# Performance work log

Measured on AMD Instinct MI355X. Metric: run time of the kernel, lower is better.

Reference implementation:

```python
import jax, jax.numpy as jnp
import numpy as np

D_MODEL = 1024
HEADS = 16
D_HEAD = D_MODEL // HEADS


def setup_inputs() -> dict:
    key = jax.random.key(0)
    ks = jax.random.split(key, 7)
    s = 1.0 / np.sqrt(D_MODEL)
    x = jax.random.normal(ks[0], (4, 2048, D_MODEL), dtype=jnp.float32)
    Wq = jax.random.uniform(ks[1], (D_MODEL, D_MODEL), jnp.float32, -s, s)
    bq = jax.random.uniform(ks[2], (D_MODEL,), jnp.float32, -s, s)
    Wk = jax.random.uniform(ks[3], (D_MODEL, D_MODEL), jnp.float32, -s, s)
    bk = jax.random.uniform(ks[4], (D_MODEL,), jnp.float32, -s, s)
    Wv = jax.random.uniform(ks[5], (D_MODEL, D_MODEL), jnp.float32, -s, s)
    bv = jax.random.uniform(ks[6], (D_MODEL,), jnp.float32, -s, s)
    return {"x": x, "Wq": Wq, "bq": bq, "Wk": Wk, "bk": bk, "Wv": Wv, "bv": bv}


def reference(x, Wq, bq, Wk, bk, Wv, bv):
    B, S, D = x.shape
    # QKV projections, split heads: [B, H, S, Dh]
    def split(t):
        return t.reshape(B, S, HEADS, D_HEAD).transpose(0, 2, 1, 3)
    q = split(x @ Wq + bq)
    k = split(x @ Wk + bk)
    v = split(x @ Wv + bv)
    scores = jnp.einsum('bhqd,bhkd->bhqk', q, k) / np.sqrt(D_HEAD).astype(jnp.float32)
    attn = jax.nn.softmax(scores, axis=-1)
    out = jnp.einsum('bhqk,bhkd->bhqd', attn, v)
    return out.transpose(0, 2, 1, 3).reshape(B, S, D)
```

## Files before the change

kernel.cpp:

```cpp
#include <hip/hip_runtime.h>

typedef _Float16 f16;
typedef __attribute__((ext_vector_type(2))) _Float16 f16x2;
typedef __attribute__((ext_vector_type(2))) __fp16   hf16x2;
typedef __attribute__((ext_vector_type(4))) _Float16 f16x4;
typedef __attribute__((ext_vector_type(8))) _Float16 f16x8;
typedef __attribute__((ext_vector_type(4))) float    f32x4;

#define D_MODEL 1024
#define HEADS   16
#define DH      64
#define SEQ     2048
#define BATCH   4
#define SSCALE  0.1803368801111204f

__device__ __forceinline__ void gload_lds16(const void* g, void* lds) {
  __builtin_amdgcn_global_load_lds(
      (const __attribute__((address_space(1))) unsigned int*)g,
      (__attribute__((address_space(3))) unsigned int*)lds, 16, 0, 0);
}

__global__ __launch_bounds__(256) void prep_kernel(const float* __restrict__ x,
                                                   const float* __restrict__ Wq,
                                                   const float* __restrict__ Wk,
                                                   const float* __restrict__ Wv,
                                                   f16* __restrict__ xb,
                                                   f16* __restrict__ wt) {
  if (blockIdx.x < 8192) {
    int i = blockIdx.x * 256 + threadIdx.x;
    float4 v = ((const float4*)x)[i];
    f16x4 h;
    h[0] = (f16)v.x; h[1] = (f16)v.y; h[2] = (f16)v.z; h[3] = (f16)v.w;
    ((f16x4*)xb)[i] = h;
    return;
  }
  int bid = blockIdx.x - 8192;
  int z = bid >> 8, rem = bid & 255;
  const float* W = z == 0 ? Wq : (z == 1 ? Wk : Wv);
  f16* out = wt + (size_t)z * D_MODEL * D_MODEL;
  __shared__ float tile[64][65];
  int n0 = (rem & 15) * 64, k0 = (rem >> 4) * 64;
  int tx = threadIdx.x & 63, ty = threadIdx.x >> 6;
#pragma unroll
  for (int r = 0; r < 16; ++r)
    tile[ty * 16 + r][tx] = W[(size_t)(k0 + ty * 16 + r) * D_MODEL + n0 + tx];
  __syncthreads();
#pragma unroll
  for (int r = 0; r < 16; ++r)
    out[(size_t)(n0 + ty * 16 + r) * D_MODEL + k0 + tx] = (f16)tile[tx][ty * 16 + r];
}

__global__ __launch_bounds__(256, 3) void qkv_gemm_kernel(
    const f16* __restrict__ xb, const f16* __restrict__ wt_all,
    const float* __restrict__ bq, const float* __restrict__ bk, const float* __restrict__ bv,
    f16* __restrict__ qout, f16* __restrict__ kout, f16* __restrict__ vtout) {
  const int z = blockIdx.z;
  const f16* wt = wt_all + (size_t)z * D_MODEL * D_MODEL;
  const float* bias = z == 0 ? bq : (z == 1 ? bk : bv);
  const int n0 = blockIdx.x * 128, m0 = blockIdx.y * 128;

  __shared__ f16 As[2][128 * 32];
  __shared__ f16 Bs[2][128 * 32];

  const int tid = threadIdx.x;
  const int lane = tid & 63, w = tid >> 6;
  const int quad = lane >> 4, l15 = lane & 15;
  const int wm = w & 1, wn = w >> 1;

  const int pce = (quad ^ ((l15 >> 1) & 3)) * 8;
  const int aoff = wm * 2048 + l15 * 32 + pce;
  const int boff = wn * 2048 + l15 * 32 + pce;

  int srow[2], scl[2];
#pragma unroll
  for (int c = 0; c < 2; ++c) {
    int slot = (w * 2 + c) * 64 + lane;
    srow[c] = slot >> 2;
    scl[c] = (slot & 3) ^ ((srow[c] >> 1) & 3);
  }

  f32x4 acc[4][4];
#pragma unroll
  for (int i = 0; i < 4; ++i)
#pragma unroll
    for (int j = 0; j < 4; ++j) acc[i][j] = (f32x4){0.f, 0.f, 0.f, 0.f};

#pragma unroll
  for (int c = 0; c < 2; ++c) {
    gload_lds16(xb + (size_t)(m0 + srow[c]) * D_MODEL + scl[c] * 8, &As[0][(w * 2 + c) * 512]);
    gload_lds16(wt + (size_t)(n0 + srow[c]) * D_MODEL + scl[c] * 8, &Bs[0][(w * 2 + c) * 512]);
  }

  f16x8 aP[4], bP[4];
  for (int it = 0; it < 32; ++it) {
    const int buf = it & 1;
    __syncthreads();
    if (it < 31) {
      const int kn = (it + 1) * 32;
#pragma unroll
      for (int c = 0; c < 2; ++c) {
        gload_lds16(xb + (size_t)(m0 + srow[c]) * D_MODEL + kn + scl[c] * 8, &As[buf ^ 1][(w * 2 + c) * 512]);
        gload_lds16(wt + (size_t)(n0 + srow[c]) * D_MODEL + kn + scl[c] * 8, &Bs[buf ^ 1][(w * 2 + c) * 512]);
      }
    }
    f16x8 aC[4], bC[4];
#pragma unroll
    for (int mt = 0; mt < 4; ++mt) aC[mt] = *(const f16x8*)(&As[buf][aoff + mt * 512]);
#pragma unroll
    for (int nt = 0; nt < 4; ++nt) bC[nt] = *(const f16x8*)(&Bs[buf][boff + nt * 512]);
    if (it) {
#pragma unroll
      for (int mt = 0; mt < 4; ++mt)
#pragma unroll
        for (int nt = 0; nt < 4; ++nt)
          acc[mt][nt] = __builtin_amdgcn_mfma_f32_16x16x32_f16(aP[mt], bP[nt], acc[mt][nt], 0, 0, 0);
    }
#pragma unroll
    for (int t = 0; t < 4; ++t) { aP[t] = aC[t]; bP[t] = bC[t]; }
  }
#pragma unroll
  for (int mt = 0; mt < 4; ++mt)
#pragma unroll
    for (int nt = 0; nt < 4; ++nt)
      acc[mt][nt] = __builtin_amdgcn_mfma_f32_16x16x32_f16(aP[mt], bP[nt], acc[mt][nt], 0, 0, 0);

  const float sc = (z == 0) ? SSCALE : 1.0f;
  float bcol[4];
#pragma unroll
  for (int nt = 0; nt < 4; ++nt) bcol[nt] = bias[n0 + wn * 64 + nt * 16 + l15];

  if (z < 2) {
    f16* out = (z == 0) ? qout : kout;
#pragma unroll
    for (int mt = 0; mt < 4; ++mt) {
      int mbase = m0 + wm * 64 + mt * 16 + quad * 4;
#pragma unroll
      for (int nt = 0; nt < 4; ++nt) {
        int n = n0 + wn * 64 + nt * 16 + l15;
        int h = n >> 6, dh = n & 63;
#pragma unroll
        for (int r = 0; r < 4; ++r) {
          int m = mbase + r;
          int b = m >> 11, s = m & 2047;
          out[((size_t)(b * HEADS + h) * SEQ + s) * DH + dh] = (f16)((acc[mt][nt][r] + bcol[nt]) * sc);
        }
      }
    }
  } else {
#pragma unroll
    for (int mt = 0; mt < 4; ++mt) {
      int mbase = m0 + wm * 64 + mt * 16 + quad * 4;
      int b = mbase >> 11, seq = mbase & 2047;
      int kt = seq >> 6;
#pragma unroll
      for (int nt = 0; nt < 4; ++nt) {
        int n = n0 + wn * 64 + nt * 16 + l15;
        int h = n >> 6, dh = n & 63;
        f16x4 v;
#pragma unroll
        for (int r = 0; r < 4; ++r) v[r] = (f16)(acc[mt][nt][r] + bcol[nt]);
        int phys = (quad * 2 + (mt >> 1)) ^ (dh & 7);
        size_t off = (((size_t)(b * HEADS + h) * 32 + kt) * 4096) + dh * 64 + phys * 8 + (mt & 1) * 4;
        *(f16x4*)(vtout + off) = v;
      }
    }
  }
}

__global__ __launch_bounds__(256, 2) void attn_kernel(
    const f16* __restrict__ q, const f16* __restrict__ k, const f16* __restrict__ vt,
    float* __restrict__ out) {
  const int bh = blockIdx.x;
  const int s0 = blockIdx.y * 256;
  const int b = bh >> 4, h = bh & 15;
  const int tid = threadIdx.x, lane = tid & 63, w = tid >> 6;
  const int quad = lane >> 4, l15 = lane & 15;

  __shared__ f16 Ks[2][64 * 64];
  __shared__ f16 Vs[2][64 * 64];

  const f16* qbase = q + ((size_t)bh * SEQ + s0 + w * 64) * DH;
  const f16* kbase = k + (size_t)bh * SEQ * DH;
  const f16* vbase = vt + (size_t)bh * DH * SEQ;

  f16x8 qf[4][2];
#pragma unroll
  for (int qt = 0; qt < 4; ++qt)
#pragma unroll
    for (int ks = 0; ks < 2; ++ks)
      qf[qt][ks] = *(const f16x8*)(qbase + (qt * 16 + l15) * DH + ks * 32 + quad * 8);

  int koff[2];
  koff[0] = l15 * 64 + ((quad ^ (l15 & 7)) * 8);
  koff[1] = l15 * 64 + (((4 + quad) ^ (l15 & 7)) * 8);
  int voff2[2];
  voff2[0] = l15 * 64 + (((quad * 2) ^ (l15 & 7)) * 8);
  voff2[1] = l15 * 64 + (((quad * 2 + 1) ^ (l15 & 7)) * 8);

  int srow[2], scl[2];
#pragma unroll
  for (int c = 0; c < 2; ++c) {
    int slot = (w * 2 + c) * 64 + lane;
    srow[c] = slot >> 3;
    scl[c] = (slot & 7) ^ (srow[c] & 7);
  }
  const int vslot = ((w * 2) * 64 + lane) * 8;
  const int vslot2 = ((w * 2 + 1) * 64 + lane) * 8;

  f32x4 lsum4[4];
#pragma unroll
  for (int qt = 0; qt < 4; ++qt) lsum4[qt] = (f32x4){0.f, 0.f, 0.f, 0.f};
  f32x4 o[4][4];
#pragma unroll
  for (int i = 0; i < 4; ++i)
#pragma unroll
    for (int j = 0; j < 4; ++j) o[i][j] = (f32x4){0.f, 0.f, 0.f, 0.f};
  const f32x4 Zero = (f32x4){0.f, 0.f, 0.f, 0.f};

#pragma unroll
  for (int c = 0; c < 2; ++c)
    gload_lds16(kbase + (size_t)srow[c] * DH + scl[c] * 8, &Ks[0][(w * 2 + c) * 512]);
  gload_lds16(vbase + vslot,  &Vs[0][(w * 2) * 512]);
  gload_lds16(vbase + vslot2, &Vs[0][(w * 2 + 1) * 512]);

  for (int kt = 0; kt < SEQ / 64; ++kt) {
    const int buf = kt & 1;
    __syncthreads();
    if (kt < SEQ / 64 - 1) {
      const int kn = (kt + 1) * 64;
#pragma unroll
      for (int c = 0; c < 2; ++c)
        gload_lds16(kbase + (size_t)(kn + srow[c]) * DH + scl[c] * 8, &Ks[buf ^ 1][(w * 2 + c) * 512]);
      gload_lds16(vbase + (kt + 1) * 4096 + vslot,  &Vs[buf ^ 1][(w * 2) * 512]);
      gload_lds16(vbase + (kt + 1) * 4096 + vslot2, &Vs[buf ^ 1][(w * 2 + 1) * 512]);
    }

    f32x4 st[4][4];
#pragma unroll
    for (int mt = 0; mt < 4; ++mt) {
      f16x8 af0 = *(const f16x8*)(&Ks[buf][koff[0] + mt * 1024]);
      f16x8 af1 = *(const f16x8*)(&Ks[buf][koff[1] + mt * 1024]);
#pragma unroll
      for (int qt = 0; qt < 4; ++qt) {
        st[mt][qt] = __builtin_amdgcn_mfma_f32_16x16x32_f16(af0, qf[qt][0], Zero, 0, 0, 0);
        st[mt][qt] = __builtin_amdgcn_mfma_f32_16x16x32_f16(af1, qf[qt][1], st[mt][qt], 0, 0, 0);
      }
    }

    f16x4 pb[4][4];
#pragma unroll
    for (int ks = 0; ks < 4; ++ks)
#pragma unroll
      for (int qt = 0; qt < 4; ++qt) {
        float e0 = __builtin_amdgcn_exp2f(st[ks][qt][0]);
        float e1 = __builtin_amdgcn_exp2f(st[ks][qt][1]);
        float e2 = __builtin_amdgcn_exp2f(st[ks][qt][2]);
        float e3 = __builtin_amdgcn_exp2f(st[ks][qt][3]);
        f32x4 ev = (f32x4){e0, e1, e2, e3};
        lsum4[qt] += ev;
        f16x2 p01 = __builtin_bit_cast(f16x2, __builtin_amdgcn_cvt_pkrtz(e0, e1));
        f16x2 p23 = __builtin_bit_cast(f16x2, __builtin_amdgcn_cvt_pkrtz(e2, e3));
        pb[ks][qt] = __builtin_shufflevector(p01, p23, 0, 1, 2, 3);
      }

#pragma unroll
    for (int half = 0; half < 2; ++half)
#pragma unroll
      for (int mt = 0; mt < 4; ++mt) {
        f16x8 v8 = *(const f16x8*)(&Vs[buf][voff2[half] + mt * 1024]);
        f16x4 vaA = __builtin_shufflevector(v8, v8, 0, 1, 2, 3);
        f16x4 vaB = __builtin_shufflevector(v8, v8, 4, 5, 6, 7);
#pragma unroll
        for (int qt = 0; qt < 4; ++qt) {
          o[mt][qt] = __builtin_amdgcn_mfma_f32_16x16x16f16(vaA, pb[half * 2][qt], o[mt][qt], 0, 0, 0);
          o[mt][qt] = __builtin_amdgcn_mfma_f32_16x16x16f16(vaB, pb[half * 2 + 1][qt], o[mt][qt], 0, 0, 0);
        }
      }
  }

#pragma unroll
  for (int qt = 0; qt < 4; ++qt) {
    float l = (lsum4[qt][0] + lsum4[qt][1]) + (lsum4[qt][2] + lsum4[qt][3]);
    l += __shfl_xor(l, 16, 64);
    l += __shfl_xor(l, 32, 64);
    float inv = 1.f / l;
    int sq = s0 + w * 64 + qt * 16 + l15;
    float* obase = out + ((size_t)b * SEQ + sq) * D_MODEL + h * DH;
#pragma unroll
    for (int mt = 0; mt < 4; ++mt) {
      f32x4 vv;
#pragma unroll
      for (int r = 0; r < 4; ++r) vv[r] = o[mt][qt][r] * inv;
      *(f32x4*)(obase + mt * 16 + quad * 4) = vv;
    }
  }
}

extern "C" void kernel_launch(void* const* d_in, const int* in_sizes, int n_in,
                              void* d_out, int out_size, void* d_ws, size_t ws_size,
                              hipStream_t stream) {
  const float* x  = (const float*)d_in[0];
  const float* Wq = (const float*)d_in[1];
  const float* bq = (const float*)d_in[2];
  const float* Wk = (const float*)d_in[3];
  const float* bk = (const float*)d_in[4];
  const float* Wv = (const float*)d_in[5];
  const float* bv = (const float*)d_in[6];
  float* out = (float*)d_out;

  char* ws = (char*)d_ws;
  f16* xb = (f16*)ws;
  f16* wt = (f16*)(ws + (size_t)16 * 1024 * 1024);
  f16* q  = (f16*)(ws + (size_t)22 * 1024 * 1024);
  f16* kk = q + (size_t)BATCH * SEQ * D_MODEL;
  f16* vt = kk + (size_t)BATCH * SEQ * D_MODEL;

  prep_kernel<<<8192 + 768, 256, 0, stream>>>(x, Wq, Wk, Wv, xb, wt);
  qkv_gemm_kernel<<<dim3(8, 64, 3), 256, 0, stream>>>(xb, wt, bq, bk, bv, q, kk, vt);
  attn_kernel<<<dim3(64, 8), 256, 0, stream>>>(q, kk, vt, out);
}
```

Before: 246.7 us.

## Triple-buffer QKV GEMM and stream attention K/V from global into registers

The QKV GEMM moves from a double-buffered to a triple-buffered LDS pipeline with explicit vmcnt waits and raw barriers, so global loads run two stages ahead. The attention kernel drops its LDS staging and block barriers. Each lane now loads its K and V MFMA fragments straight from global into registers, prefetching the next tile while computing, and uses s_setprio around the MFMA blocks. The V^T output layout is changed to match the new per-lane register load pattern. This removes LDS traffic and synchronization but adds register pressure and repeats K/V global loads across the four waves.

New measurement: 290.8 us. 17.9% more time.

```diff
diff --git a/kernel.cpp b/kernel.cpp
--- a/kernel.cpp
+++ b/kernel.cpp
@@ -59,8 +59,8 @@
   const float* bias = z == 0 ? bq : (z == 1 ? bk : bv);
   const int n0 = blockIdx.x * 128, m0 = blockIdx.y * 128;
 
-  __shared__ f16 As[2][128 * 32];
-  __shared__ f16 Bs[2][128 * 32];
+  __shared__ f16 As[3][128 * 32];
+  __shared__ f16 Bs[3][128 * 32];
 
   const int tid = threadIdx.x;
   const int lane = tid & 63, w = tid >> 6;
@@ -86,21 +86,27 @@
     for (int j = 0; j < 4; ++j) acc[i][j] = (f32x4){0.f, 0.f, 0.f, 0.f};
 
 #pragma unroll
-  for (int c = 0; c < 2; ++c) {
-    gload_lds16(xb + (size_t)(m0 + srow[c]) * D_MODEL + scl[c] * 8, &As[0][(w * 2 + c) * 512]);
-    gload_lds16(wt + (size_t)(n0 + srow[c]) * D_MODEL + scl[c] * 8, &Bs[0][(w * 2 + c) * 512]);
-  }
+  for (int t = 0; t < 2; ++t)
+#pragma unroll
+    for (int c = 0; c < 2; ++c) {
+      gload_lds16(xb + (size_t)(m0 + srow[c]) * D_MODEL + t * 32 + scl[c] * 8, &As[t][(w * 2 + c) * 512]);
+      gload_lds16(wt + (size_t)(n0 + srow[c]) * D_MODEL + t * 32 + scl[c] * 8, &Bs[t][(w * 2 + c) * 512]);
+    }
 
   f16x8 aP[4], bP[4];
+  int buf = 0;
   for (int it = 0; it < 32; ++it) {
-    const int buf = it & 1;
-    __syncthreads();
-    if (it < 31) {
-      const int kn = (it + 1) * 32;
+    if (it == 31) { asm volatile("s_waitcnt vmcnt(0)" ::: "memory"); }
+    else          { asm volatile("s_waitcnt vmcnt(4)" ::: "memory"); }
+    __builtin_amdgcn_s_barrier();
+    __builtin_amdgcn_sched_barrier(0);
+    if (it < 30) {
+      const int sb = buf ? buf - 1 : 2;
+      const int kn = (it + 2) * 32;
 #pragma unroll
       for (int c = 0; c < 2; ++c) {
-        gload_lds16(xb + (size_t)(m0 + srow[c]) * D_MODEL + kn + scl[c] * 8, &As[buf ^ 1][(w * 2 + c) * 512]);
-        gload_lds16(wt + (size_t)(n0 + srow[c]) * D_MODEL + kn + scl[c] * 8, &Bs[buf ^ 1][(w * 2 + c) * 512]);
+        gload_lds16(xb + (size_t)(m0 + srow[c]) * D_MODEL + kn + scl[c] * 8, &As[sb][(w * 2 + c) * 512]);
+        gload_lds16(wt + (size_t)(n0 + srow[c]) * D_MODEL + kn + scl[c] * 8, &Bs[sb][(w * 2 + c) * 512]);
       }
     }
     f16x8 aC[4], bC[4];
@@ -117,6 +123,7 @@
     }
 #pragma unroll
     for (int t = 0; t < 4; ++t) { aP[t] = aC[t]; bP[t] = bC[t]; }
+    buf = (buf == 2) ? 0 : buf + 1;
   }
 #pragma unroll
   for (int mt = 0; mt < 4; ++mt)
@@ -159,8 +166,9 @@
         f16x4 v;
 #pragma unroll
         for (int r = 0; r < 4; ++r) v[r] = (f16)(acc[mt][nt][r] + bcol[nt]);
-        int phys = (quad * 2 + (mt >> 1)) ^ (dh & 7);
-        size_t off = (((size_t)(b * HEADS + h) * 32 + kt) * 4096) + dh * 64 + phys * 8 + (mt & 1) * 4;
+        size_t off = (((size_t)(b * HEADS + h) * 32 + kt) * 4096)
+                   + (((mt >> 1) * 4 + (dh >> 4)) * 64 + quad * 16 + (dh & 15)) * 8
+                   + (mt & 1) * 4;
         *(f16x4*)(vtout + off) = v;
       }
     }
@@ -176,12 +184,9 @@
   const int tid = threadIdx.x, lane = tid & 63, w = tid >> 6;
   const int quad = lane >> 4, l15 = lane & 15;
 
-  __shared__ f16 Ks[2][64 * 64];
-  __shared__ f16 Vs[2][64 * 64];
-
   const f16* qbase = q + ((size_t)bh * SEQ + s0 + w * 64) * DH;
-  const f16* kbase = k + (size_t)bh * SEQ * DH;
-  const f16* vbase = vt + (size_t)bh * DH * SEQ;
+  const f16* kptr = k + (size_t)bh * SEQ * DH + l15 * DH + quad * 8;
+  const f16* vptr = vt + (size_t)bh * DH * SEQ + lane * 8;
 
   f16x8 qf[4][2];
 #pragma unroll
@@ -190,23 +195,6 @@
     for (int ks = 0; ks < 2; ++ks)
       qf[qt][ks] = *(const f16x8*)(qbase + (qt * 16 + l15) * DH + ks * 32 + quad * 8);
 
-  int koff[2];
-  koff[0] = l15 * 64 + ((quad ^ (l15 & 7)) * 8);
-  koff[1] = l15 * 64 + (((4 + quad) ^ (l15 & 7)) * 8);
-  int voff2[2];
-  voff2[0] = l15 * 64 + (((quad * 2) ^ (l15 & 7)) * 8);
-  voff2[1] = l15 * 64 + (((quad * 2 + 1) ^ (l15 & 7)) * 8);
-
-  int srow[2], scl[2];
-#pragma unroll
-  for (int c = 0; c < 2; ++c) {
-    int slot = (w * 2 + c) * 64 + lane;
-    srow[c] = slot >> 3;
-    scl[c] = (slot & 7) ^ (srow[c] & 7);
-  }
-  const int vslot = ((w * 2) * 64 + lane) * 8;
-  const int vslot2 = ((w * 2 + 1) * 64 + lane) * 8;
-
   f32x4 lsum4[4];
 #pragma unroll
   for (int qt = 0; qt < 4; ++qt) lsum4[qt] = (f32x4){0.f, 0.f, 0.f, 0.f};
@@ -217,65 +205,70 @@
     for (int j = 0; j < 4; ++j) o[i][j] = (f32x4){0.f, 0.f, 0.f, 0.f};
   const f32x4 Zero = (f32x4){0.f, 0.f, 0.f, 0.f};
 
-#pragma unroll
-  for (int c = 0; c < 2; ++c)
-    gload_lds16(kbase + (size_t)srow[c] * DH + scl[c] * 8, &Ks[0][(w * 2 + c) * 512]);
-  gload_lds16(vbase + vslot,  &Vs[0][(w * 2) * 512]);
-  gload_lds16(vbase + vslot2, &Vs[0][(w * 2 + 1) * 512]);
-
+  f16x8 kf[4][2], vf[2][4];
+#pragma unroll
+  for (int mt = 0; mt < 4; ++mt) {
+    kf[mt][0] = *(const f16x8*)(kptr + mt * 16 * DH);
+    kf[mt][1] = *(const f16x8*)(kptr + mt * 16 * DH + 32);
+  }
+#pragma unroll
+  for (int hf = 0; hf < 2; ++hf)
+#pragma unroll
+    for (int mt = 0; mt < 4; ++mt)
+      vf[hf][mt] = *(const f16x8*)(vptr + (hf * 4 + mt) * 512);
+
+#pragma unroll 1
   for (int kt = 0; kt < SEQ / 64; ++kt) {
-    const int buf = kt & 1;
-    __syncthreads();
-    if (kt < SEQ / 64 - 1) {
-      const int kn = (kt + 1) * 64;
-#pragma unroll
-      for (int c = 0; c < 2; ++c)
-        gload_lds16(kbase + (size_t)(kn + srow[c]) * DH + scl[c] * 8, &Ks[buf ^ 1][(w * 2 + c) * 512]);
-      gload_lds16(vbase + (kt + 1) * 4096 + vslot,  &Vs[buf ^ 1][(w * 2) * 512]);
-      gload_lds16(vbase + (kt + 1) * 4096 + vslot2, &Vs[buf ^ 1][(w * 2 + 1) * 512]);
-    }
-
-    f32x4 st[4][4];
-#pragma unroll
-    for (int mt = 0; mt < 4; ++mt) {
-      f16x8 af0 = *(const f16x8*)(&Ks[buf][koff[0] + mt * 1024]);
-      f16x8 af1 = *(const f16x8*)(&Ks[buf][koff[1] + mt * 1024]);
-#pragma unroll
-      for (int qt = 0; qt < 4; ++qt) {
-        st[mt][qt] = __builtin_amdgcn_mfma_f32_16x16x32_f16(af0, qf[qt][0], Zero, 0, 0, 0);
-        st[mt][qt] = __builtin_amdgcn_mfma_f32_16x16x32_f16(af1, qf[qt][1], st[mt][qt], 0, 0, 0);
-      }
-    }
-
-    f16x4 pb[4][4];
-#pragma unroll
-    for (int ks = 0; ks < 4; ++ks)
-#pragma unroll
-      for (int qt = 0; qt < 4; ++qt) {
-        float e0 = __builtin_amdgcn_exp2f(st[ks][qt][0]);
-        float e1 = __builtin_amdgcn_exp2f(st[ks][qt][1]);
-        float e2 = __builtin_amdgcn_exp2f(st[ks][qt][2]);
-        float e3 = __builtin_amdgcn_exp2f(st[ks][qt][3]);
-        f32x4 ev = (f32x4){e0, e1, e2, e3};
-        lsum4[qt] += ev;
-        f16x2 p01 = __builtin_bit_cast(f16x2, __builtin_amdgcn_cvt_pkrtz(e0, e1));
-        f16x2 p23 = __builtin_bit_cast(f16x2, __builtin_amdgcn_cvt_pkrtz(e2, e3));
-        pb[ks][qt] = __builtin_shufflevector(p01, p23, 0, 1, 2, 3);
-      }
-
-#pragma unroll
-    for (int half = 0; half < 2; ++half)
-#pragma unroll
-      for (int mt = 0; mt < 4; ++mt) {
-        f16x8 v8 = *(const f16x8*)(&Vs[buf][voff2[half] + mt * 1024]);
+    const f16* kn = kptr + (size_t)(kt + 1) * 64 * DH;
+    const f16* vn = vptr + (size_t)(kt + 1) * 4096;
+
+#pragma unroll
+    for (int seg = 0; seg < 2; ++seg) {
+      f16x4 pb[2][4];
+#pragma unroll
+      for (int m2 = 0; m2 < 2; ++m2) {
+        const int mt = seg * 2 + m2;
+        f16x8 a0 = kf[mt][0], a1 = kf[mt][1];
+        if (kt < SEQ / 64 - 1) {
+          kf[mt][0] = *(const f16x8*)(kn + mt * 16 * DH);
+          kf[mt][1] = *(const f16x8*)(kn + mt * 16 * DH + 32);
+        }
+        f32x4 st[4];
+        __builtin_amdgcn_s_setprio(1);
+#pragma unroll
+        for (int qt = 0; qt < 4; ++qt) {
+          st[qt] = __builtin_amdgcn_mfma_f32_16x16x32_f16(a0, qf[qt][0], Zero, 0, 0, 0);
+          st[qt] = __builtin_amdgcn_mfma_f32_16x16x32_f16(a1, qf[qt][1], st[qt], 0, 0, 0);
+        }
+        __builtin_amdgcn_s_setprio(0);
+#pragma unroll
+        for (int qt = 0; qt < 4; ++qt) {
+          float e0 = __builtin_amdgcn_exp2f(st[qt][0]);
+          float e1 = __builtin_amdgcn_exp2f(st[qt][1]);
+          float e2 = __builtin_amdgcn_exp2f(st[qt][2]);
+          float e3 = __builtin_amdgcn_exp2f(st[qt][3]);
+          lsum4[qt] += (f32x4){e0, e1, e2, e3};
+          f16x2 p01 = __builtin_bit_cast(f16x2, __builtin_amdgcn_cvt_pkrtz(e0, e1));
+          f16x2 p23 = __builtin_bit_cast(f16x2, __builtin_amdgcn_cvt_pkrtz(e2, e3));
+          pb[m2][qt] = __builtin_shufflevector(p01, p23, 0, 1, 2, 3);
+        }
+      }
+#pragma unroll
+      for (int mtv = 0; mtv < 4; ++mtv) {
+        f16x8 v8 = vf[seg][mtv];
+        if (kt < SEQ / 64 - 1)
+          vf[seg][mtv] = *(const f16x8*)(vn + (seg * 4 + mtv) * 512);
         f16x4 vaA = __builtin_shufflevector(v8, v8, 0, 1, 2, 3);
         f16x4 vaB = __builtin_shufflevector(v8, v8, 4, 5, 6, 7);
+        __builtin_amdgcn_s_setprio(1);
 #pragma unroll
         for (int qt = 0; qt < 4; ++qt) {
-          o[mt][qt] = __builtin_amdgcn_mfma_f32_16x16x16f16(vaA, pb[half * 2][qt], o[mt][qt], 0, 0, 0);
-          o[mt][qt] = __builtin_amdgcn_mfma_f32_16x16x16f16(vaB, pb[half * 2 + 1][qt], o[mt][qt], 0, 0, 0);
-        }
-      }
+          o[mtv][qt] = __builtin_amdgcn_mfma_f32_16x16x16f16(vaA, pb[0][qt], o[mtv][qt], 0, 0, 0);
+          o[mtv][qt] = __builtin_amdgcn_mfma_f32_16x16x16f16(vaB, pb[1][qt], o[mtv][qt], 0, 0, 0);
+        }
+        __builtin_amdgcn_s_setprio(0);
+      }
+    }
   }
 
 #pragma unroll
```

## Triple-buffer QKV GEMM loads, swap operands for Q/K, vectorize epilogue stores

Applied to the files above, without the earlier changes.

The QKV projection GEMM moves from double to triple-buffered LDS staging, prefetching two k-steps ahead with explicit vmcnt waits and raw barriers in place of __syncthreads. For Q and K it swaps the A/B operands (weights as A, activations as B), so each lane holds 4 contiguous head-dim values and can write f16x4 vectors instead of scalar f16 stores. The V epilogue combines two f16x4 stores into one f16x8 store. This targets global-load latency and the scattered scalar stores in the epilogue, at the cost of 50% more LDS, which may limit occupancy at 3 blocks per CU.

New measurement: 250.7 us. About the same (+1.7%).

```diff
diff --git a/kernel.cpp b/kernel.cpp
--- a/kernel.cpp
+++ b/kernel.cpp
@@ -59,8 +59,11 @@
   const float* bias = z == 0 ? bq : (z == 1 ? bk : bv);
   const int n0 = blockIdx.x * 128, m0 = blockIdx.y * 128;
 
-  __shared__ f16 As[2][128 * 32];
-  __shared__ f16 Bs[2][128 * 32];
+  const f16* srcA = (z < 2) ? wt : xb;  const int baseA = (z < 2) ? n0 : m0;
+  const f16* srcB = (z < 2) ? xb : wt;  const int baseB = (z < 2) ? m0 : n0;
+
+  __shared__ f16 As[3][128 * 32];
+  __shared__ f16 Bs[3][128 * 32];
 
   const int tid = threadIdx.x;
   const int lane = tid & 63, w = tid >> 6;
@@ -86,21 +89,27 @@
     for (int j = 0; j < 4; ++j) acc[i][j] = (f32x4){0.f, 0.f, 0.f, 0.f};
 
 #pragma unroll
-  for (int c = 0; c < 2; ++c) {
-    gload_lds16(xb + (size_t)(m0 + srow[c]) * D_MODEL + scl[c] * 8, &As[0][(w * 2 + c) * 512]);
-    gload_lds16(wt + (size_t)(n0 + srow[c]) * D_MODEL + scl[c] * 8, &Bs[0][(w * 2 + c) * 512]);
-  }
+  for (int t = 0; t < 2; ++t)
+#pragma unroll
+    for (int c = 0; c < 2; ++c) {
+      gload_lds16(srcA + (size_t)(baseA + srow[c]) * D_MODEL + t * 32 + scl[c] * 8, &As[t][(w * 2 + c) * 512]);
+      gload_lds16(srcB + (size_t)(baseB + srow[c]) * D_MODEL + t * 32 + scl[c] * 8, &Bs[t][(w * 2 + c) * 512]);
+    }
 
   f16x8 aP[4], bP[4];
+  int buf = 0;
   for (int it = 0; it < 32; ++it) {
-    const int buf = it & 1;
-    __syncthreads();
-    if (it < 31) {
-      const int kn = (it + 1) * 32;
+    if (it == 31) { asm volatile("s_waitcnt vmcnt(0)" ::: "memory"); }
+    else          { asm volatile("s_waitcnt vmcnt(4)" ::: "memory"); }
+    __builtin_amdgcn_s_barrier();
+    __builtin_amdgcn_sched_barrier(0);
+    if (it < 30) {
+      const int sb = buf ? buf - 1 : 2;
+      const int kn = (it + 2) * 32;
 #pragma unroll
       for (int c = 0; c < 2; ++c) {
-        gload_lds16(xb + (size_t)(m0 + srow[c]) * D_MODEL + kn + scl[c] * 8, &As[buf ^ 1][(w * 2 + c) * 512]);
-        gload_lds16(wt + (size_t)(n0 + srow[c]) * D_MODEL + kn + scl[c] * 8, &Bs[buf ^ 1][(w * 2 + c) * 512]);
+        gload_lds16(srcA + (size_t)(baseA + srow[c]) * D_MODEL + kn + scl[c] * 8, &As[sb][(w * 2 + c) * 512]);
+        gload_lds16(srcB + (size_t)(baseB + srow[c]) * D_MODEL + kn + scl[c] * 8, &Bs[sb][(w * 2 + c) * 512]);
       }
     }
     f16x8 aC[4], bC[4];
@@ -117,6 +126,7 @@
     }
 #pragma unroll
     for (int t = 0; t < 4; ++t) { aP[t] = aC[t]; bP[t] = bC[t]; }
+    buf = (buf == 2) ? 0 : buf + 1;
   }
 #pragma unroll
   for (int mt = 0; mt < 4; ++mt)
@@ -124,44 +134,48 @@
     for (int nt = 0; nt < 4; ++nt)
       acc[mt][nt] = __builtin_amdgcn_mfma_f32_16x16x32_f16(aP[mt], bP[nt], acc[mt][nt], 0, 0, 0);
 
-  const float sc = (z == 0) ? SSCALE : 1.0f;
-  float bcol[4];
-#pragma unroll
-  for (int nt = 0; nt < 4; ++nt) bcol[nt] = bias[n0 + wn * 64 + nt * 16 + l15];
-
   if (z < 2) {
-    f16* out = (z == 0) ? qout : kout;
-#pragma unroll
-    for (int mt = 0; mt < 4; ++mt) {
-      int mbase = m0 + wm * 64 + mt * 16 + quad * 4;
-#pragma unroll
-      for (int nt = 0; nt < 4; ++nt) {
-        int n = n0 + wn * 64 + nt * 16 + l15;
-        int h = n >> 6, dh = n & 63;
-#pragma unroll
-        for (int r = 0; r < 4; ++r) {
-          int m = mbase + r;
-          int b = m >> 11, s = m & 2047;
-          out[((size_t)(b * HEADS + h) * SEQ + s) * DH + dh] = (f16)((acc[mt][nt][r] + bcol[nt]) * sc);
-        }
+    const float sc = (z == 0) ? SSCALE : 1.0f;
+    f16* outp = (z == 0) ? qout : kout;
+    const int hbase = (n0 + wm * 64) >> 6;
+    f32x4 bb[4];
+#pragma unroll
+    for (int mt = 0; mt < 4; ++mt)
+      bb[mt] = *(const f32x4*)(bias + n0 + wm * 64 + mt * 16 + quad * 4);
+#pragma unroll
+    for (int nt = 0; nt < 4; ++nt) {
+      int m = m0 + wn * 64 + nt * 16 + l15;
+      int b = m >> 11, s = m & 2047;
+      f16* rowp = outp + ((size_t)(b * HEADS + hbase) * SEQ + s) * DH;
+#pragma unroll
+      for (int mt = 0; mt < 4; ++mt) {
+        f16x4 hv;
+#pragma unroll
+        for (int r = 0; r < 4; ++r) hv[r] = (f16)((acc[mt][nt][r] + bb[mt][r]) * sc);
+        *(f16x4*)(rowp + mt * 16 + quad * 4) = hv;
       }
     }
   } else {
-#pragma unroll
-    for (int mt = 0; mt < 4; ++mt) {
-      int mbase = m0 + wm * 64 + mt * 16 + quad * 4;
-      int b = mbase >> 11, seq = mbase & 2047;
-      int kt = seq >> 6;
-#pragma unroll
-      for (int nt = 0; nt < 4; ++nt) {
-        int n = n0 + wn * 64 + nt * 16 + l15;
-        int h = n >> 6, dh = n & 63;
-        f16x4 v;
-#pragma unroll
-        for (int r = 0; r < 4; ++r) v[r] = (f16)(acc[mt][nt][r] + bcol[nt]);
-        int phys = (quad * 2 + (mt >> 1)) ^ (dh & 7);
-        size_t off = (((size_t)(b * HEADS + h) * 32 + kt) * 4096) + dh * 64 + phys * 8 + (mt & 1) * 4;
-        *(f16x4*)(vtout + off) = v;
+    float bcol[4];
+#pragma unroll
+    for (int nt = 0; nt < 4; ++nt) bcol[nt] = bias[n0 + wn * 64 + nt * 16 + l15];
+    const int mb = m0 + wm * 64;
+    const int b = mb >> 11, seq = mb & 2047;
+    const int kt = seq >> 6;
+#pragma unroll
+    for (int nt = 0; nt < 4; ++nt) {
+      int n = n0 + wn * 64 + nt * 16 + l15;
+      int h = n >> 6, dh = n & 63;
+      size_t tb = (((size_t)(b * HEADS + h) * 32 + kt) * 4096) + dh * 64;
+#pragma unroll
+      for (int p = 0; p < 2; ++p) {
+        int phys = (quad * 2 + p) ^ (dh & 7);
+        f16x8 hv;
+#pragma unroll
+        for (int r = 0; r < 4; ++r) hv[r]     = (f16)(acc[2 * p][nt][r]     + bcol[nt]);
+#pragma unroll
+        for (int r = 0; r < 4; ++r) hv[4 + r] = (f16)(acc[2 * p + 1][nt][r] + bcol[nt]);
+        *(f16x8*)(vtout + tb + phys * 8) = hv;
       }
     }
   }
```

## Triple-buffer QKV GEMM with swizzled block order and split attention launch

Applied to the files above, without the earlier changes.

The QKV GEMM moves from a double-buffered to a triple-buffered LDS pipeline. It prefetches two k-steps ahead and uses explicit vmcnt waits with raw barriers in place of __syncthreads. The 3D grid is flattened into a 1D grid with a grouped block-index remap, meant to improve L2 reuse of the x and weight tiles. The attention launch is split into two half-grid launches via a bh offset, which adds launch overhead without an obvious parallelism gain. The extra LDS buffer raises shared memory use and may affect occupancy at 3 blocks per CU.

Result: slower. 264.5 us (+7.2%).

```diff
diff --git a/kernel.cpp b/kernel.cpp
--- a/kernel.cpp
+++ b/kernel.cpp
@@ -54,13 +54,17 @@
     const f16* __restrict__ xb, const f16* __restrict__ wt_all,
     const float* __restrict__ bq, const float* __restrict__ bk, const float* __restrict__ bv,
     f16* __restrict__ qout, f16* __restrict__ kout, f16* __restrict__ vtout) {
-  const int z = blockIdx.z;
+  const int bid = blockIdx.x;
+  const int j = bid & 7, t = bid >> 3;
+  const int by = j * 8 + (t & 7);
+  const int bx = (t >> 3) & 7;
+  const int z  = t >> 6;
   const f16* wt = wt_all + (size_t)z * D_MODEL * D_MODEL;
   const float* bias = z == 0 ? bq : (z == 1 ? bk : bv);
-  const int n0 = blockIdx.x * 128, m0 = blockIdx.y * 128;
-
-  __shared__ f16 As[2][128 * 32];
-  __shared__ f16 Bs[2][128 * 32];
+  const int n0 = bx * 128, m0 = by * 128;
+
+  __shared__ f16 As[3][128 * 32];
+  __shared__ f16 Bs[3][128 * 32];
 
   const int tid = threadIdx.x;
   const int lane = tid & 63, w = tid >> 6;
@@ -83,24 +87,30 @@
 #pragma unroll
   for (int i = 0; i < 4; ++i)
 #pragma unroll
-    for (int j = 0; j < 4; ++j) acc[i][j] = (f32x4){0.f, 0.f, 0.f, 0.f};
-
-#pragma unroll
-  for (int c = 0; c < 2; ++c) {
-    gload_lds16(xb + (size_t)(m0 + srow[c]) * D_MODEL + scl[c] * 8, &As[0][(w * 2 + c) * 512]);
-    gload_lds16(wt + (size_t)(n0 + srow[c]) * D_MODEL + scl[c] * 8, &Bs[0][(w * 2 + c) * 512]);
-  }
+    for (int jj = 0; jj < 4; ++jj) acc[i][jj] = (f32x4){0.f, 0.f, 0.f, 0.f};
+
+#pragma unroll
+  for (int tt = 0; tt < 2; ++tt)
+#pragma unroll
+    for (int c = 0; c < 2; ++c) {
+      gload_lds16(xb + (size_t)(m0 + srow[c]) * D_MODEL + tt * 32 + scl[c] * 8, &As[tt][(w * 2 + c) * 512]);
+      gload_lds16(wt + (size_t)(n0 + srow[c]) * D_MODEL + tt * 32 + scl[c] * 8, &Bs[tt][(w * 2 + c) * 512]);
+    }
 
   f16x8 aP[4], bP[4];
+  int buf = 0;
   for (int it = 0; it < 32; ++it) {
-    const int buf = it & 1;
-    __syncthreads();
-    if (it < 31) {
-      const int kn = (it + 1) * 32;
+    if (it == 31) { asm volatile("s_waitcnt vmcnt(0)" ::: "memory"); }
+    else          { asm volatile("s_waitcnt vmcnt(4)" ::: "memory"); }
+    __builtin_amdgcn_s_barrier();
+    __builtin_amdgcn_sched_barrier(0);
+    if (it < 30) {
+      const int sb = buf ? buf - 1 : 2;
+      const int kn = (it + 2) * 32;
 #pragma unroll
       for (int c = 0; c < 2; ++c) {
-        gload_lds16(xb + (size_t)(m0 + srow[c]) * D_MODEL + kn + scl[c] * 8, &As[buf ^ 1][(w * 2 + c) * 512]);
-        gload_lds16(wt + (size_t)(n0 + srow[c]) * D_MODEL + kn + scl[c] * 8, &Bs[buf ^ 1][(w * 2 + c) * 512]);
+        gload_lds16(xb + (size_t)(m0 + srow[c]) * D_MODEL + kn + scl[c] * 8, &As[sb][(w * 2 + c) * 512]);
+        gload_lds16(wt + (size_t)(n0 + srow[c]) * D_MODEL + kn + scl[c] * 8, &Bs[sb][(w * 2 + c) * 512]);
       }
     }
     f16x8 aC[4], bC[4];
@@ -116,7 +126,8 @@
           acc[mt][nt] = __builtin_amdgcn_mfma_f32_16x16x32_f16(aP[mt], bP[nt], acc[mt][nt], 0, 0, 0);
     }
 #pragma unroll
-    for (int t = 0; t < 4; ++t) { aP[t] = aC[t]; bP[t] = bC[t]; }
+    for (int tt = 0; tt < 4; ++tt) { aP[tt] = aC[tt]; bP[tt] = bC[tt]; }
+    buf = (buf == 2) ? 0 : buf + 1;
   }
 #pragma unroll
   for (int mt = 0; mt < 4; ++mt)
@@ -169,8 +180,8 @@
 
 __global__ __launch_bounds__(256, 2) void attn_kernel(
     const f16* __restrict__ q, const f16* __restrict__ k, const f16* __restrict__ vt,
-    float* __restrict__ out) {
-  const int bh = blockIdx.x;
+    float* __restrict__ out, int bh0) {
+  const int bh = blockIdx.x + bh0;
   const int s0 = blockIdx.y * 256;
   const int b = bh >> 4, h = bh & 15;
   const int tid = threadIdx.x, lane = tid & 63, w = tid >> 6;
@@ -214,7 +225,7 @@
 #pragma unroll
   for (int i = 0; i < 4; ++i)
 #pragma unroll
-    for (int j = 0; j < 4; ++j) o[i][j] = (f32x4){0.f, 0.f, 0.f, 0.f};
+    for (int jj = 0; jj < 4; ++jj) o[i][jj] = (f32x4){0.f, 0.f, 0.f, 0.f};
   const f32x4 Zero = (f32x4){0.f, 0.f, 0.f, 0.f};
 
 #pragma unroll
@@ -316,6 +327,7 @@
   f16* vt = kk + (size_t)BATCH * SEQ * D_MODEL;
 
   prep_kernel<<<8192 + 768, 256, 0, stream>>>(x, Wq, Wk, Wv, xb, wt);
-  qkv_gemm_kernel<<<dim3(8, 64, 3), 256, 0, stream>>>(xb, wt, bq, bk, bv, q, kk, vt);
-  attn_kernel<<<dim3(64, 8), 256, 0, stream>>>(q, kk, vt, out);
-}
+  qkv_gemm_kernel<<<1536, 256, 0, stream>>>(xb, wt, bq, bk, bv, q, kk, vt);
+  attn_kernel<<<dim3(32, 8), 256, 0, stream>>>(q, kk, vt, out, 0);
+  attn_kernel<<<dim3(32, 8), 256, 0, stream>>>(q, kk, vt, out, 32);
+}
```
